# Kernel optimization log

Hardware: AMD Instinct MI355X
Metric: run time of the kernel (lower is better)

Reference implementation:

```python
import jax, jax.numpy as jnp
import numpy as np

B, T, E, H, C = 32, 128, 256, 256, 16

def setup_inputs() -> dict:
    key = jax.random.key(0)
    ks = jax.random.split(key, 16)
    def p(k, shape, scale=0.05):
        return jax.random.normal(k, shape, dtype=jnp.float32) * scale
    return {
        "x": jax.random.normal(ks[0], (B, T, E), dtype=jnp.float32),
        "W_in": p(ks[1], (H, E)), "b_in": p(ks[2], (H,)),
        "Wih": p(ks[3], (3 * H, H)), "bih": p(ks[4], (3 * H,)),
        "Whh": p(ks[5], (3 * H, H)), "bhh": p(ks[6], (3 * H,)),
        "Wa": p(ks[7], (H, H)), "ba": p(ks[8], (H,)),
        "Ua": p(ks[9], (H, H)), "ub": p(ks[10], (H,)),
        "va_w": p(ks[11], (1, H)), "va_b": p(ks[12], (1,)),
        "Wo": p(ks[13], (C, 2 * H)), "bo": p(ks[14], (C,)),
    }

def reference(x, W_in, b_in, Wih, bih, Whh, bhh, Wa, ba, Ua, ub, va_w, va_b, Wo, bo):
    # linear_in (+ Identity activation): x -> [B,T,H]
    xp = x @ W_in.T + b_in
    xp_t = jnp.transpose(xp, (1, 0, 2))          # [T,B,H], time-major
    # Precompute per-step GRU input projections and attention key projections
    xw = xp_t @ Wih.T + bih                      # [T,B,3H]
    uax = xp_t @ Ua.T + ub                       # [T,B,H]
    ts = jnp.arange(T)

    def gru_step(h, xw_t):
        # PyTorch GRU cell: gate order r, z, n
        hw = h @ Whh.T + bhh                     # [B,3H]
        xr, xz, xn = jnp.split(xw_t, 3, axis=-1)
        hr, hz, hn = jnp.split(hw, 3, axis=-1)
        r = jax.nn.sigmoid(xr + hr)
        z = jax.nn.sigmoid(xz + hz)
        n = jnp.tanh(xn + r * hn)
        return (1.0 - z) * n + z * h

    def outer_step(h_prev, i):
        # Re-run RNN over prefix x[:, :i+1] starting from the CARRIED hidden,
        # exactly as the torch loop does (hidden is not reset between iters).
        def inner(h, inp):
            t, xw_t = inp
            hn = gru_step(h, xw_t)
            h = jnp.where(t <= i, hn, h)         # freeze past the prefix end
            return h, h
        h_last, outs = jax.lax.scan(inner, h_prev, (ts, xw))  # outs [T,B,H]
        # Bahdanau attention: query = rnn outputs, keys = linear_in outputs
        s = jnp.tanh(outs @ Wa.T + ba + uax)     # [T,B,H]
        scores = jnp.squeeze(s @ va_w.T, -1) + va_b  # [T,B]
        scores = jnp.where((ts <= i)[:, None], scores, -1e9)
        w = jax.nn.softmax(scores, axis=0)       # softmax over prefix positions
        context = jnp.einsum('tb,tbh->bh', w, xp_t)
        cats = jnp.concatenate([h_last, context], axis=-1)  # [B,2H]
        return h_last, cats @ Wo.T + bo          # logits [B,C]

    h0 = jnp.zeros((x.shape[0], H), dtype=x.dtype)
    _, logits = jax.lax.scan(outer_step, h0, ts)  # [T,B,C]
    return jax.nn.sigmoid(jnp.transpose(logits, (1, 0, 2)))  # [B,T,C]
```

## Files before the change

kernel.cpp:

```cpp
#include <hip/hip_runtime.h>

constexpr int NB = 32;
constexpr int NT = 128;
constexpr int NE = 256;
constexpr int NH = 256;
constexpr int NC = 16;

typedef _Float16 f16;
typedef f16 f16x2 __attribute__((ext_vector_type(2)));
typedef f16 f16x8 __attribute__((ext_vector_type(8)));

__device__ __forceinline__ float sigmoidf_(float x) {
    return 1.f / (1.f + __expf(-x));
}
__device__ __forceinline__ float tanhf_(float x) {
    x = fminf(fmaxf(x, -15.f), 15.f);
    float e = __expf(-2.f * x);
    return (1.f - e) / (1.f + e);
}
__device__ __forceinline__ float dot4_(float4 a, float4 b) {
    return a.x * b.x + a.y * b.y + a.z * b.z + a.w * b.w;
}
#if __has_builtin(__builtin_amdgcn_fdot2)
__device__ __forceinline__ float fdot2_(f16x2 a, f16x2 b, float c) {
    return __builtin_amdgcn_fdot2(a, b, c, false);
}
#else
__device__ __forceinline__ float fdot2_(f16x2 a, f16x2 b, float c) {
    return (float)a[0] * (float)b[0] + (float)a[1] * (float)b[1] + c;
}
#endif
#define PAIR(v, k) __builtin_shufflevector((v), (v), (k), (k) + 1)

__global__ __launch_bounds__(256) void k_lin_in(
    const float* __restrict__ x, const float* __restrict__ W_in,
    const float* __restrict__ b_in, float* __restrict__ xp) {
    const int tb = blockIdx.x;
    const int t = tb >> 5, b = tb & 31;
    const int tid = threadIdx.x;
    __shared__ __align__(16) float xl[NE];
    xl[tid] = x[(b * NT + t) * NE + tid];
    __syncthreads();
    const float* __restrict__ wr = W_in + tid * NE;
    float acc = b_in[tid];
#pragma unroll 8
    for (int k = 0; k < NE; k += 4)
        acc += dot4_(*(const float4*)(wr + k), *(const float4*)(xl + k));
    xp[tb * NH + tid] = acc;
}

__global__ __launch_bounds__(256) void k_proj(
    const float* __restrict__ xp, const float* __restrict__ Wih,
    const float* __restrict__ bih, const float* __restrict__ Ua,
    const float* __restrict__ ub, float* __restrict__ xw,
    float* __restrict__ uax) {
    const int tb = blockIdx.x;
    const int tid = threadIdx.x;
    __shared__ __align__(16) float xl[NH];
    xl[tid] = xp[tb * NH + tid];
    __syncthreads();
    const float* __restrict__ wr = Wih + tid * NH;
    const float* __restrict__ wz = Wih + (NH + tid) * NH;
    const float* __restrict__ wn = Wih + (2 * NH + tid) * NH;
    const float* __restrict__ wu = Ua + tid * NH;
    float ar = bih[tid], az = bih[NH + tid], an = bih[2 * NH + tid], au = ub[tid];
#pragma unroll 4
    for (int k = 0; k < NH; k += 4) {
        float4 xv = *(const float4*)(xl + k);
        ar += dot4_(*(const float4*)(wr + k), xv);
        az += dot4_(*(const float4*)(wz + k), xv);
        an += dot4_(*(const float4*)(wn + k), xv);
        au += dot4_(*(const float4*)(wu + k), xv);
    }
    float* xwp = xw + tb * (3 * NH);
    xwp[tid] = ar;
    xwp[NH + tid] = az;
    xwp[2 * NH + tid] = an;
    uax[tb * NH + tid] = au;
}

__global__ __launch_bounds__(256) void k_pack(
    const float* __restrict__ Whh, const float* __restrict__ Wa,
    f16x8* __restrict__ Wpk, f16x8* __restrict__ Wak) {
    const int id = blockIdx.x * 256 + threadIdx.x;
    if (id < 32 * 768) {
        const int kc = id / 768, row = id % 768;
        const float* src = Whh + row * NH + kc * 8;
        f16x8 v;
#pragma unroll
        for (int m = 0; m < 8; ++m) v[m] = (f16)src[m];
        Wpk[id] = v;
    } else {
        const int id2 = id - 32 * 768;
        const int kc = id2 >> 8, row = id2 & 255;
        const float* src = Wa + row * NH + kc * 8;
        f16x8 v;
#pragma unroll
        for (int m = 0; m < 8; ++m) v[m] = (f16)src[m];
        Wak[id2] = v;
    }
}

__global__ __launch_bounds__(512) void k_chain(
    const f16x8* __restrict__ Wpk, const float* __restrict__ bhh,
    const float* __restrict__ xw, float* __restrict__ Hc) {
    const int b = blockIdx.x;
    const int tid = threadIdx.x;
    const int j = tid >> 1, c = tid & 1;

    __shared__ __align__(16) f16x8 nW[32 * 256];
    __shared__ __align__(16) f16 hb[2][272];

#pragma unroll
    for (int it = 0; it < 16; ++it) {
        const int id = it * 512 + tid;
        nW[id] = Wpk[(size_t)(id >> 8) * 768 + 512 + (id & 255)];
    }

    f16x8 rw[16], zw[16];
    {
        const f16x8* __restrict__ rbase = Wpk + (size_t)(c * 16) * 768 + j;
#pragma unroll
        for (int s = 0; s < 16; ++s) {
            rw[s] = rbase[(size_t)s * 768];
            zw[s] = rbase[(size_t)s * 768 + 256];
        }
    }
    const float bhr = bhh[j], bhz = bhh[NH + j], bhn = bhh[2 * NH + j];
    if (tid < NH) hb[0][(tid < 128) ? tid : 136 + (tid - 128)] = (f16)0.f;
    float hprev = 0.f;
    int cur = 0;
    const int jpad = (j < 128) ? j : 136 + (j - 128);
    const f16* __restrict__ nbase = (const f16*)(nW + (c * 16) * 256 + j);
    __syncthreads();

#pragma unroll 1
    for (int i = 0; i < NT; ++i) {
#pragma unroll 1
        for (int t = 0; t <= i; ++t) {
            const float* __restrict__ xwp = xw + (size_t)(t * NB + b) * (3 * NH);
            const float xr = xwp[j], xz = xwp[NH + j], xn = xwp[2 * NH + j];

            const f16* hc = hb[cur] + c * 136;
            float ar = 0.f, az = 0.f, an = 0.f;
#pragma unroll
            for (int s = 0; s < 16; ++s) {
                const f16x8 hv = *(const f16x8*)(hc + s * 8);
                const f16x8 nv = *(const f16x8*)(nbase + (size_t)s * 2048);
                const f16x2 h0 = PAIR(hv, 0), h1 = PAIR(hv, 2),
                            h2 = PAIR(hv, 4), h3 = PAIR(hv, 6);
                ar = fdot2_(PAIR(rw[s], 0), h0, ar);
                ar = fdot2_(PAIR(rw[s], 2), h1, ar);
                ar = fdot2_(PAIR(rw[s], 4), h2, ar);
                ar = fdot2_(PAIR(rw[s], 6), h3, ar);
                az = fdot2_(PAIR(zw[s], 0), h0, az);
                az = fdot2_(PAIR(zw[s], 2), h1, az);
                az = fdot2_(PAIR(zw[s], 4), h2, az);
                az = fdot2_(PAIR(zw[s], 6), h3, az);
                an = fdot2_(PAIR(nv, 0), h0, an);
                an = fdot2_(PAIR(nv, 2), h1, an);
                an = fdot2_(PAIR(nv, 4), h2, an);
                an = fdot2_(PAIR(nv, 6), h3, an);
            }
            ar += __shfl_xor(ar, 1);
            az += __shfl_xor(az, 1);
            an += __shfl_xor(an, 1);
            const float r = sigmoidf_(xr + ar + bhr);
            const float z = sigmoidf_(xz + az + bhz);
            const float n = tanhf_(xn + r * (an + bhn));
            const float hnew = (1.f - z) * n + z * hprev;
            hprev = hnew;
            if (c == 0) {
                hb[cur ^ 1][jpad] = (f16)hnew;
                if (t == i) Hc[((size_t)i * NB + b) * NH + j] = hnew;
            }
            cur ^= 1;
            __syncthreads();
        }
    }
}

__global__ __attribute__((amdgpu_waves_per_eu(2, 2))) __launch_bounds__(512)
void k_attn(
    const float* __restrict__ Hc, const float* __restrict__ xw,
    const float* __restrict__ uax, const float* __restrict__ xp,
    const f16x8* __restrict__ Wpk, const f16x8* __restrict__ Wak,
    const float* __restrict__ bhh, const float* __restrict__ ba,
    const float* __restrict__ va_w, const float* __restrict__ Wo,
    const float* __restrict__ bo, float* __restrict__ out) {
    const int b  = blockIdx.x >> 3;
    const int bk = blockIdx.x & 7;
    const int tid = threadIdx.x;
    const int col = tid >> 1, c = tid & 1;
    const int lane = tid & 63, wid = tid >> 6;

    __shared__ __align__(16) float S[16][NH];
    __shared__ __align__(16) f16 Sh[16][NH];
    __shared__ float red1[8][16];
    __shared__ float mL[16], lL[16], aL[16], eL[16];
    __shared__ float redH[8][256];

    const float bhr = bhh[col], bhz = bhh[NH + col], bhn = bhh[2 * NH + col];
    const float ba_j = ba[col], va_j = va_w[col];
    float ctx[16];
#pragma unroll
    for (int u = 0; u < 16; ++u) {
        const int ic = bk + 8 * u;
        const float hv = (ic == 0) ? 0.f : Hc[((size_t)(ic - 1) * NB + b) * NH + col];
        if (c == 0) { S[u][col] = hv; Sh[u][col] = (f16)hv; }
        ctx[u] = 0.f;
    }
    if (tid < 16) { mL[tid] = -1e30f; lL[tid] = 0.f; }
    __syncthreads();

    const int imax = bk + 8 * 15;
#pragma unroll 1
    for (int t = 0; t <= imax; ++t) {
        const size_t base = (size_t)(t * NB + b);
        const float xr = xw[base * 3 * NH + col];
        const float xz = xw[base * 3 * NH + NH + col];
        const float xn = xw[base * 3 * NH + 2 * NH + col];
        const float ux = uax[base * NH + col];
        const float xpt = xp[base * NH + col];

        float ar[16], az[16], an[16];
#pragma unroll
        for (int u = 0; u < 16; ++u) { ar[u] = 0.f; az[u] = 0.f; an[u] = 0.f; }
#pragma unroll 2
        for (int kk = 0; kk < 16; ++kk) {
            const int kc = kk * 2 + c;
            const f16x8 wR = Wpk[kc * 768 + col];
            const f16x8 wZ = Wpk[kc * 768 + 256 + col];
            const f16x8 wN = Wpk[kc * 768 + 512 + col];
#pragma unroll
            for (int u = 0; u < 16; ++u) {
                if (bk + 8 * u < t) continue;
                const f16x8 hv = *(const f16x8*)&Sh[u][kc * 8];
                const f16x2 h0 = PAIR(hv, 0), h1 = PAIR(hv, 2),
                            h2 = PAIR(hv, 4), h3 = PAIR(hv, 6);
                ar[u] = fdot2_(PAIR(wR, 0), h0, ar[u]);
                ar[u] = fdot2_(PAIR(wR, 2), h1, ar[u]);
                ar[u] = fdot2_(PAIR(wR, 4), h2, ar[u]);
                ar[u] = fdot2_(PAIR(wR, 6), h3, ar[u]);
                az[u] = fdot2_(PAIR(wZ, 0), h0, az[u]);
                az[u] = fdot2_(PAIR(wZ, 2), h1, az[u]);
                az[u] = fdot2_(PAIR(wZ, 4), h2, az[u]);
                az[u] = fdot2_(PAIR(wZ, 6), h3, az[u]);
                an[u] = fdot2_(PAIR(wN, 0), h0, an[u]);
                an[u] = fdot2_(PAIR(wN, 2), h1, an[u]);
                an[u] = fdot2_(PAIR(wN, 4), h2, an[u]);
                an[u] = fdot2_(PAIR(wN, 6), h3, an[u]);
            }
        }
        float hn[16];
#pragma unroll
        for (int u = 0; u < 16; ++u) {
            if (bk + 8 * u < t) continue;
            float arf = ar[u] + __shfl_xor(ar[u], 1);
            float azf = az[u] + __shfl_xor(az[u], 1);
            float anf = an[u] + __shfl_xor(an[u], 1);
            const float r = sigmoidf_(xr + arf + bhr);
            const float z = sigmoidf_(xz + azf + bhz);
            const float n = tanhf_(xn + r * (anf + bhn));
            hn[u] = (1.f - z) * n + z * S[u][col];
        }
        __syncthreads();
#pragma unroll
        for (int u = 0; u < 16; ++u) {
            if (bk + 8 * u < t) continue;
            if (c == 0) { S[u][col] = hn[u]; Sh[u][col] = (f16)hn[u]; }
        }
        __syncthreads();

        float sc[16];
#pragma unroll
        for (int u = 0; u < 16; ++u) sc[u] = 0.f;
#pragma unroll 2
        for (int kk = 0; kk < 16; ++kk) {
            const int kc = kk * 2 + c;
            const f16x8 wA = Wak[kc * 256 + col];
#pragma unroll
            for (int u = 0; u < 16; ++u) {
                if (bk + 8 * u < t) continue;
                const f16x8 hv = *(const f16x8*)&Sh[u][kc * 8];
                sc[u] = fdot2_(PAIR(wA, 0), PAIR(hv, 0), sc[u]);
                sc[u] = fdot2_(PAIR(wA, 2), PAIR(hv, 2), sc[u]);
                sc[u] = fdot2_(PAIR(wA, 4), PAIR(hv, 4), sc[u]);
                sc[u] = fdot2_(PAIR(wA, 6), PAIR(hv, 6), sc[u]);
            }
        }
#pragma unroll
        for (int u = 0; u < 16; ++u) {
            if (bk + 8 * u < t) continue;
            const float sv = sc[u] + __shfl_xor(sc[u], 1);
            float p = (c == 0) ? va_j * tanhf_(sv + ba_j + ux) : 0.f;
#pragma unroll
            for (int off = 32; off; off >>= 1) p += __shfl_xor(p, off);
            if (lane == 0) red1[wid][u] = p;
        }
        __syncthreads();
        if (tid < 16 && bk + 8 * tid >= t) {
            float s = 0.f;
#pragma unroll
            for (int w = 0; w < 8; ++w) s += red1[w][tid];
            const float mo = mL[tid];
            const float mn = fmaxf(mo, s);
            const float e  = __expf(s - mn);
            const float al = __expf(mo - mn);
            lL[tid] = lL[tid] * al + e;
            mL[tid] = mn; aL[tid] = al; eL[tid] = e;
        }
        __syncthreads();
#pragma unroll
        for (int u = 0; u < 16; ++u) {
            if (bk + 8 * u < t) continue;
            ctx[u] = ctx[u] * aL[u] + eL[u] * xpt;
        }
    }

#pragma unroll 1
    for (int u = 0; u < 16; ++u) {
        const float hl = S[u][col];
        const float cx = ctx[u] / lL[u];
#pragma unroll
        for (int cls = 0; cls < NC; ++cls) {
            float p = Wo[cls * (2 * NH) + col] * hl + Wo[cls * (2 * NH) + NH + col] * cx;
            p = (c == 0) ? p : 0.f;
#pragma unroll
            for (int off = 32; off; off >>= 1) p += __shfl_xor(p, off);
            if (lane == 0) redH[wid][u * 16 + cls] = p;
        }
    }
    __syncthreads();
    if (tid < 256) {
        const int u = tid >> 4, cls = tid & 15;
        const int ic = bk + 8 * u;
        float lg = bo[cls];
#pragma unroll
        for (int w = 0; w < 8; ++w) lg += redH[w][tid];
        out[((size_t)b * NT + ic) * NC + cls] = sigmoidf_(lg);
    }
}

extern "C" void kernel_launch(void* const* d_in, const int* in_sizes, int n_in,
                              void* d_out, int out_size, void* d_ws, size_t ws_size,
                              hipStream_t stream) {
    (void)in_sizes; (void)n_in; (void)out_size; (void)ws_size;
    const float* x    = (const float*)d_in[0];
    const float* W_in = (const float*)d_in[1];
    const float* b_in = (const float*)d_in[2];
    const float* Wih  = (const float*)d_in[3];
    const float* bih  = (const float*)d_in[4];
    const float* Whh  = (const float*)d_in[5];
    const float* bhh  = (const float*)d_in[6];
    const float* Wa   = (const float*)d_in[7];
    const float* ba   = (const float*)d_in[8];
    const float* Ua   = (const float*)d_in[9];
    const float* ub   = (const float*)d_in[10];
    const float* va_w = (const float*)d_in[11];
    const float* Wo   = (const float*)d_in[13];
    const float* bo   = (const float*)d_in[14];
    float* out = (float*)d_out;

    float* ws  = (float*)d_ws;
    float* xp  = ws;
    float* xw  = xp  + (size_t)NT * NB * NH;
    float* uax = xw  + (size_t)NT * NB * 3 * NH;
    float* Hc  = uax + (size_t)NT * NB * NH;
    f16x8* Wpk = (f16x8*)(Hc + (size_t)NT * NB * NH);
    f16x8* Wak = Wpk + 32 * 768;

    hipLaunchKernelGGL(k_lin_in, dim3(NT * NB), dim3(256), 0, stream, x, W_in, b_in, xp);
    hipLaunchKernelGGL(k_proj,   dim3(NT * NB), dim3(256), 0, stream, xp, Wih, bih, Ua, ub, xw, uax);
    hipLaunchKernelGGL(k_pack,   dim3(128),     dim3(256), 0, stream, Whh, Wa, Wpk, Wak);
    hipLaunchKernelGGL(k_chain,  dim3(NB),      dim3(512), 0, stream, Wpk, bhh, xw, Hc);
    hipLaunchKernelGGL(k_attn,   dim3(NB * 8),  dim3(512), 0, stream,
                       Hc, xw, uax, xp, Wpk, Wak, bhh, ba, va_w, Wo, bo, out);
}
```

Before: 14.94 ms.

## Re-tile GRU chain kernel to 4 outputs per thread with 8-way K split

The sequential GRU chain kernel is restructured. Each thread now computes 4 hidden units over a 32-wide K slice, and an 8-lane shuffle reduction combines the partial sums. A new packed Whh layout is generated for this mapping. Part of the z/n weights is streamed from global/L2 each step instead of being held in registers or LDS, and the r/z recurrent biases are folded into the precomputed input projection. The aim is fewer LDS hidden-state reads and vectorized xw loads, at the cost of more shuffles and per-step global weight traffic.

```diff
diff --git a/kernel.cpp b/kernel.cpp
--- a/kernel.cpp
+++ b/kernel.cpp
@@ -8,6 +8,7 @@
 
 typedef _Float16 f16;
 typedef f16 f16x2 __attribute__((ext_vector_type(2)));
+typedef f16 f16x4 __attribute__((ext_vector_type(4)));
 typedef f16 f16x8 __attribute__((ext_vector_type(8)));
 
 __device__ __forceinline__ float sigmoidf_(float x) {
@@ -31,6 +32,17 @@
 }
 #endif
 #define PAIR(v, k) __builtin_shufflevector((v), (v), (k), (k) + 1)
+
+__device__ __forceinline__ float dotp_(const f16x8* w, const f16x8* hv, float acc) {
+#pragma unroll
+    for (int cc = 0; cc < 4; ++cc) {
+        acc = fdot2_(PAIR(w[cc], 0), PAIR(hv[cc], 0), acc);
+        acc = fdot2_(PAIR(w[cc], 2), PAIR(hv[cc], 2), acc);
+        acc = fdot2_(PAIR(w[cc], 4), PAIR(hv[cc], 4), acc);
+        acc = fdot2_(PAIR(w[cc], 6), PAIR(hv[cc], 6), acc);
+    }
+    return acc;
+}
 
 __global__ __launch_bounds__(256) void k_lin_in(
     const float* __restrict__ x, const float* __restrict__ W_in,
@@ -52,8 +64,8 @@
 __global__ __launch_bounds__(256) void k_proj(
     const float* __restrict__ xp, const float* __restrict__ Wih,
     const float* __restrict__ bih, const float* __restrict__ Ua,
-    const float* __restrict__ ub, float* __restrict__ xw,
-    float* __restrict__ uax) {
+    const float* __restrict__ ub, const float* __restrict__ bhh,
+    float* __restrict__ xw, float* __restrict__ uax) {
     const int tb = blockIdx.x;
     const int tid = threadIdx.x;
     __shared__ __align__(16) float xl[NH];
@@ -73,106 +85,172 @@
         au += dot4_(*(const float4*)(wu + k), xv);
     }
     float* xwp = xw + tb * (3 * NH);
-    xwp[tid] = ar;
-    xwp[NH + tid] = az;
+    xwp[tid] = ar + bhh[tid];
+    xwp[NH + tid] = az + bhh[NH + tid];
     xwp[2 * NH + tid] = an;
     uax[tb * NH + tid] = au;
 }
 
 __global__ __launch_bounds__(256) void k_pack(
     const float* __restrict__ Whh, const float* __restrict__ Wa,
-    f16x8* __restrict__ Wpk, f16x8* __restrict__ Wak) {
+    f16x8* __restrict__ Wpk, f16x8* __restrict__ Wak,
+    f16x8* __restrict__ Wpk2) {
     const int id = blockIdx.x * 256 + threadIdx.x;
-    if (id < 32 * 768) {
+    if (id < 24576) {
         const int kc = id / 768, row = id % 768;
         const float* src = Whh + row * NH + kc * 8;
         f16x8 v;
 #pragma unroll
         for (int m = 0; m < 8; ++m) v[m] = (f16)src[m];
         Wpk[id] = v;
-    } else {
-        const int id2 = id - 32 * 768;
+    } else if (id < 32768) {
+        const int id2 = id - 24576;
         const int kc = id2 >> 8, row = id2 & 255;
         const float* src = Wa + row * NH + kc * 8;
         f16x8 v;
 #pragma unroll
         for (int m = 0; m < 8; ++m) v[m] = (f16)src[m];
         Wak[id2] = v;
+    } else {
+        const int id3 = id - 32768;
+        const int cc = id3 & 3;
+        const int g = (id3 >> 2) & 63;
+        const int rem = id3 >> 8;
+        const int p = rem % 12;
+        const int q = rem / 12;
+        const int row = (p >> 2) * 256 + 4 * g + (p & 3);
+        const int kb = 32 * q + 8 * cc;
+        const float* src = Whh + row * NH + kb;
+        f16x8 v;
+#pragma unroll
+        for (int m = 0; m < 8; ++m) v[m] = (f16)src[m];
+        Wpk2[id3] = v;
     }
 }
 
 __global__ __launch_bounds__(512) void k_chain(
-    const f16x8* __restrict__ Wpk, const float* __restrict__ bhh,
+    const f16x8* __restrict__ Wpk2, const float* __restrict__ bhh,
     const float* __restrict__ xw, float* __restrict__ Hc) {
     const int b = blockIdx.x;
     const int tid = threadIdx.x;
-    const int j = tid >> 1, c = tid & 1;
-
-    __shared__ __align__(16) f16x8 nW[32 * 256];
-    __shared__ __align__(16) f16 hb[2][272];
-
-#pragma unroll
-    for (int it = 0; it < 16; ++it) {
-        const int id = it * 512 + tid;
-        nW[id] = Wpk[(size_t)(id >> 8) * 768 + 512 + (id & 255)];
-    }
-
-    f16x8 rw[16], zw[16];
-    {
-        const f16x8* __restrict__ rbase = Wpk + (size_t)(c * 16) * 768 + j;
-#pragma unroll
-        for (int s = 0; s < 16; ++s) {
-            rw[s] = rbase[(size_t)s * 768];
-            zw[s] = rbase[(size_t)s * 768 + 256];
-        }
-    }
-    const float bhr = bhh[j], bhz = bhh[NH + j], bhn = bhh[2 * NH + j];
-    if (tid < NH) hb[0][(tid < 128) ? tid : 136 + (tid - 128)] = (f16)0.f;
-    float hprev = 0.f;
+    const int g = tid >> 3;
+    const int q = tid & 7;
+
+    const f16x8* __restrict__ Wt = Wpk2 + q * 3072 + g * 4;
+
+    __shared__ __align__(16) f16x8 sW[8 * 512];
+    __shared__ __align__(16) f16 hb[2][320];
+
+#pragma unroll
+    for (int sc = 0; sc < 8; ++sc)
+        sW[sc * 512 + tid] = Wt[(2 + (sc >> 2)) * 256 + (sc & 3)];
+
+    f16x8 rw0[4], rw1[4];
+#pragma unroll
+    for (int cc = 0; cc < 4; ++cc) { rw0[cc] = Wt[cc]; rw1[cc] = Wt[256 + cc]; }
+
+    const float4 bn4 = *(const float4*)(bhh + 2 * NH + 4 * g);
+    if (tid < 320) hb[0][tid] = (f16)0.f;
+    float hp0 = 0.f, hp1 = 0.f, hp2 = 0.f, hp3 = 0.f;
     int cur = 0;
-    const int jpad = (j < 128) ? j : 136 + (j - 128);
-    const f16* __restrict__ nbase = (const f16*)(nW + (c * 16) * 256 + j);
     __syncthreads();
 
 #pragma unroll 1
     for (int i = 0; i < NT; ++i) {
 #pragma unroll 1
         for (int t = 0; t <= i; ++t) {
-            const float* __restrict__ xwp = xw + (size_t)(t * NB + b) * (3 * NH);
-            const float xr = xwp[j], xz = xwp[NH + j], xn = xwp[2 * NH + j];
-
-            const f16* hc = hb[cur] + c * 136;
-            float ar = 0.f, az = 0.f, an = 0.f;
-#pragma unroll
-            for (int s = 0; s < 16; ++s) {
-                const f16x8 hv = *(const f16x8*)(hc + s * 8);
-                const f16x8 nv = *(const f16x8*)(nbase + (size_t)s * 2048);
-                const f16x2 h0 = PAIR(hv, 0), h1 = PAIR(hv, 2),
-                            h2 = PAIR(hv, 4), h3 = PAIR(hv, 6);
-                ar = fdot2_(PAIR(rw[s], 0), h0, ar);
-                ar = fdot2_(PAIR(rw[s], 2), h1, ar);
-                ar = fdot2_(PAIR(rw[s], 4), h2, ar);
-                ar = fdot2_(PAIR(rw[s], 6), h3, ar);
-                az = fdot2_(PAIR(zw[s], 0), h0, az);
-                az = fdot2_(PAIR(zw[s], 2), h1, az);
-                az = fdot2_(PAIR(zw[s], 4), h2, az);
-                az = fdot2_(PAIR(zw[s], 6), h3, az);
-                an = fdot2_(PAIR(nv, 0), h0, an);
-                an = fdot2_(PAIR(nv, 2), h1, an);
-                an = fdot2_(PAIR(nv, 4), h2, an);
-                an = fdot2_(PAIR(nv, 6), h3, an);
-            }
-            ar += __shfl_xor(ar, 1);
-            az += __shfl_xor(az, 1);
-            an += __shfl_xor(an, 1);
-            const float r = sigmoidf_(xr + ar + bhr);
-            const float z = sigmoidf_(xz + az + bhz);
-            const float n = tanhf_(xn + r * (an + bhn));
-            const float hnew = (1.f - z) * n + z * hprev;
-            hprev = hnew;
-            if (c == 0) {
-                hb[cur ^ 1][jpad] = (f16)hnew;
-                if (t == i) Hc[((size_t)i * NB + b) * NH + j] = hnew;
+            f16x8 wa[4], wb_[4];
+#pragma unroll
+            for (int cc = 0; cc < 4; ++cc) {
+                wa[cc] = Wt[4 * 256 + cc];
+                wb_[cc] = Wt[5 * 256 + cc];
+            }
+            const float* __restrict__ xq = xw + (size_t)(t * NB + b) * (3 * NH);
+            const float4 xr4 = *(const float4*)(xq + 4 * g);
+            const float4 xz4 = *(const float4*)(xq + NH + 4 * g);
+            const float4 xn4 = *(const float4*)(xq + 2 * NH + 4 * g);
+
+            const f16* hc = hb[cur] + 40 * q;
+            f16x8 hvv[4];
+#pragma unroll
+            for (int m = 0; m < 4; ++m) hvv[m] = *(const f16x8*)(hc + 8 * m);
+
+            float ar0 = dotp_(rw0, hvv, 0.f);
+            float ar1 = dotp_(rw1, hvv, 0.f);
+            f16x8 lw[4];
+#pragma unroll
+            for (int cc = 0; cc < 4; ++cc) lw[cc] = sW[cc * 512 + tid];
+            float ar2 = dotp_(lw, hvv, 0.f);
+#pragma unroll
+            for (int cc = 0; cc < 4; ++cc) lw[cc] = sW[(4 + cc) * 512 + tid];
+            float ar3 = dotp_(lw, hvv, 0.f);
+
+            f16x8 wc[4], wd[4];
+#pragma unroll
+            for (int cc = 0; cc < 4; ++cc) {
+                wc[cc] = Wt[6 * 256 + cc];
+                wd[cc] = Wt[7 * 256 + cc];
+            }
+            float az0 = dotp_(wa, hvv, 0.f);
+            float az1 = dotp_(wb_, hvv, 0.f);
+
+#pragma unroll
+            for (int cc = 0; cc < 4; ++cc) {
+                wa[cc] = Wt[8 * 256 + cc];
+                wb_[cc] = Wt[9 * 256 + cc];
+            }
+            float az2 = dotp_(wc, hvv, 0.f);
+            float az3 = dotp_(wd, hvv, 0.f);
+
+#pragma unroll
+            for (int cc = 0; cc < 4; ++cc) {
+                wc[cc] = Wt[10 * 256 + cc];
+                wd[cc] = Wt[11 * 256 + cc];
+            }
+            float an0 = dotp_(wa, hvv, 0.f);
+            float an1 = dotp_(wb_, hvv, 0.f);
+            float an2 = dotp_(wc, hvv, 0.f);
+            float an3 = dotp_(wd, hvv, 0.f);
+
+            ar0 += __shfl_xor(ar0, 1); ar0 += __shfl_xor(ar0, 2); ar0 += __shfl_xor(ar0, 4);
+            ar1 += __shfl_xor(ar1, 1); ar1 += __shfl_xor(ar1, 2); ar1 += __shfl_xor(ar1, 4);
+            ar2 += __shfl_xor(ar2, 1); ar2 += __shfl_xor(ar2, 2); ar2 += __shfl_xor(ar2, 4);
+            ar3 += __shfl_xor(ar3, 1); ar3 += __shfl_xor(ar3, 2); ar3 += __shfl_xor(ar3, 4);
+            az0 += __shfl_xor(az0, 1); az0 += __shfl_xor(az0, 2); az0 += __shfl_xor(az0, 4);
+            az1 += __shfl_xor(az1, 1); az1 += __shfl_xor(az1, 2); az1 += __shfl_xor(az1, 4);
+            az2 += __shfl_xor(az2, 1); az2 += __shfl_xor(az2, 2); az2 += __shfl_xor(az2, 4);
+            az3 += __shfl_xor(az3, 1); az3 += __shfl_xor(az3, 2); az3 += __shfl_xor(az3, 4);
+            an0 += __shfl_xor(an0, 1); an0 += __shfl_xor(an0, 2); an0 += __shfl_xor(an0, 4);
+            an1 += __shfl_xor(an1, 1); an1 += __shfl_xor(an1, 2); an1 += __shfl_xor(an1, 4);
+            an2 += __shfl_xor(an2, 1); an2 += __shfl_xor(an2, 2); an2 += __shfl_xor(an2, 4);
+            an3 += __shfl_xor(an3, 1); an3 += __shfl_xor(an3, 2); an3 += __shfl_xor(an3, 4);
+
+            const float r0 = sigmoidf_(xr4.x + ar0);
+            const float r1 = sigmoidf_(xr4.y + ar1);
+            const float r2 = sigmoidf_(xr4.z + ar2);
+            const float r3 = sigmoidf_(xr4.w + ar3);
+            const float z0 = sigmoidf_(xz4.x + az0);
+            const float z1 = sigmoidf_(xz4.y + az1);
+            const float z2 = sigmoidf_(xz4.z + az2);
+            const float z3 = sigmoidf_(xz4.w + az3);
+            const float n0 = tanhf_(xn4.x + r0 * (an0 + bn4.x));
+            const float n1 = tanhf_(xn4.y + r1 * (an1 + bn4.y));
+            const float n2 = tanhf_(xn4.z + r2 * (an2 + bn4.z));
+            const float n3 = tanhf_(xn4.w + r3 * (an3 + bn4.w));
+            const float h0 = (1.f - z0) * n0 + z0 * hp0; hp0 = h0;
+            const float h1 = (1.f - z1) * n1 + z1 * hp1; hp1 = h1;
+            const float h2 = (1.f - z2) * n2 + z2 * hp2; hp2 = h2;
+            const float h3 = (1.f - z3) * n3 + z3 * hp3; hp3 = h3;
+
+            if (q == 0) {
+                f16x4 hv4;
+                hv4[0] = (f16)h0; hv4[1] = (f16)h1;
+                hv4[2] = (f16)h2; hv4[3] = (f16)h3;
+                *(f16x4*)(hb[cur ^ 1] + 40 * (g >> 3) + 4 * (g & 7)) = hv4;
+                if (t == i) {
+                    float4 o; o.x = h0; o.y = h1; o.z = h2; o.w = h3;
+                    *(float4*)(Hc + ((size_t)i * NB + b) * NH + 4 * g) = o;
+                }
             }
             cur ^= 1;
             __syncthreads();
@@ -200,7 +278,7 @@
     __shared__ float mL[16], lL[16], aL[16], eL[16];
     __shared__ float redH[8][256];
 
-    const float bhr = bhh[col], bhz = bhh[NH + col], bhn = bhh[2 * NH + col];
+    const float bhn = bhh[2 * NH + col];
     const float ba_j = ba[col], va_j = va_w[col];
     float ctx[16];
 #pragma unroll
@@ -259,8 +337,8 @@
             float arf = ar[u] + __shfl_xor(ar[u], 1);
             float azf = az[u] + __shfl_xor(az[u], 1);
             float anf = an[u] + __shfl_xor(an[u], 1);
-            const float r = sigmoidf_(xr + arf + bhr);
-            const float z = sigmoidf_(xz + azf + bhz);
+            const float r = sigmoidf_(xr + arf);
+            const float z = sigmoidf_(xz + azf);
             const float n = tanhf_(xn + r * (anf + bhn));
             hn[u] = (1.f - z) * n + z * S[u][col];
         }
@@ -368,12 +446,13 @@
     float* uax = xw  + (size_t)NT * NB * 3 * NH;
     float* Hc  = uax + (size_t)NT * NB * NH;
     f16x8* Wpk = (f16x8*)(Hc + (size_t)NT * NB * NH);
-    f16x8* Wak = Wpk + 32 * 768;
+    f16x8* Wak = Wpk + 24576;
+    f16x8* Wpk2 = Wak + 8192;
 
     hipLaunchKernelGGL(k_lin_in, dim3(NT * NB), dim3(256), 0, stream, x, W_in, b_in, xp);
-    hipLaunchKernelGGL(k_proj,   dim3(NT * NB), dim3(256), 0, stream, xp, Wih, bih, Ua, ub, xw, uax);
-    hipLaunchKernelGGL(k_pack,   dim3(128),     dim3(256), 0, stream, Whh, Wa, Wpk, Wak);
-    hipLaunchKernelGGL(k_chain,  dim3(NB),      dim3(512), 0, stream, Wpk, bhh, xw, Hc);
+    hipLaunchKernelGGL(k_proj,   dim3(NT * NB), dim3(256), 0, stream, xp, Wih, bih, Ua, ub, bhh, xw, uax);
+    hipLaunchKernelGGL(k_pack,   dim3(224),     dim3(256), 0, stream, Whh, Wa, Wpk, Wak, Wpk2);
+    hipLaunchKernelGGL(k_chain,  dim3(NB),      dim3(512), 0, stream, Wpk2, bhh, xw, Hc);
     hipLaunchKernelGGL(k_attn,   dim3(NB * 8),  dim3(512), 0, stream,
                        Hc, xw, uax, xp, Wpk, Wak, bhh, ba, va_w, Wo, bo, out);
 }
```

After: 21.34 ms. 42.8% more time.
